# Optimization experiments

Measured on AMD Instinct MI355X. Metric: run time of the kernel, lower is better.

Reference implementation:

```python
import jax, jax.numpy as jnp
import numpy as np

B, C, CI, H, W = 8, 256, 128, 48, 48


def conv1x1(x, w, b):
    # x: (B,C,H,W), w: (CI,C), b: (CI,)
    return jnp.einsum('bchw,oc->bohw', x, w) + b[None, :, None, None]


def setup_inputs() -> dict:
    key = jax.random.key(0)
    ks = jax.random.split(key, 14)
    s = 1.0 / np.sqrt(C)
    d = {
        'x_1': jax.random.normal(ks[0], (B, C, H, W), jnp.float32),
        'x_2': jax.random.normal(ks[1], (B, C, H, W), jnp.float32),
    }
    names = ['v1', 'k1', 'q1', 'v2', 'k2', 'q2']
    for i, n in enumerate(names):
        d['w_' + n] = jax.random.uniform(ks[2 + 2 * i], (CI, C), jnp.float32, -s, s)
        d['b_' + n] = jax.random.uniform(ks[3 + 2 * i], (CI,), jnp.float32, -s, s)
    return d


def reference(x_1, x_2, w_v1, b_v1, w_k1, b_k1, w_q1, b_q1,
              w_v2, b_v2, w_k2, b_k2, w_q2, b_q2):
    b, ci, h, w = x_1.shape[0], w_v1.shape[0], x_1.shape[2], x_1.shape[3]
    n = h * w
    V1 = conv1x1(x_1, w_v1, b_v1).reshape(b, ci, n)
    K1 = conv1x1(x_1, w_k1, b_k1).reshape(b, ci, n)
    Q1 = conv1x1(x_1, w_q1, b_q1).reshape(b, ci, n)
    V2 = conv1x1(x_2, w_v2, b_v2).reshape(b, ci, n)
    K2 = conv1x1(x_2, w_k2, b_k2).reshape(b, ci, n)
    Q2 = conv1x1(x_2, w_q2, b_q2).reshape(b, ci, n)
    # sigmoid-gated cross attention, (B, N, N)
    R12 = jax.nn.sigmoid(jnp.einsum('bcn,bcm->bnm', Q1, K2))
    R21 = jax.nn.sigmoid(jnp.einsum('bcn,bcm->bnm', Q2, K1))
    Fu1 = jnp.einsum('bnm,bcm->bcn', R12, V2).reshape(b, ci, h, w)
    Fu2 = jnp.einsum('bnm,bcm->bcn', R21, V1).reshape(b, ci, h, w)
    y_1 = jnp.concatenate([x_1, Fu1], axis=1)
    y_2 = jnp.concatenate([x_2, Fu2], axis=1)
    return (y_1, y_2)
```

## Files before the change

kernel.cpp:

```cpp
#include <hip/hip_runtime.h>
#include <hip/hip_bf16.h>


typedef __bf16 bf16;
typedef __bf16 bf16x8 __attribute__((ext_vector_type(8)));
typedef __bf16 bf16x4 __attribute__((ext_vector_type(4)));
typedef float f32x4 __attribute__((ext_vector_type(4)));

#define NB 8
#define NC 256
#define NCI 128
#define NHW 2304
#define NT32 72
#define KPAD 136
#define VPAD 72

__global__ __launch_bounds__(256) void wconv_kernel(
    const float* __restrict__ w0, const float* __restrict__ w1,
    const float* __restrict__ w2, const float* __restrict__ w3,
    const float* __restrict__ w4, const float* __restrict__ w5,
    bf16* __restrict__ dst)
{
    int idx = (blockIdx.x * 256 + threadIdx.x) * 8;
    int m = idx >> 15;
    int off = idx & 32767;
    const float* w = (m == 0) ? w0 : (m == 1) ? w1 : (m == 2) ? w2
                   : (m == 3) ? w3 : (m == 4) ? w4 : w5;
    f32x4 a0 = *(const f32x4*)(w + off);
    f32x4 a1 = *(const f32x4*)(w + off + 4);
    bf16x8 o;
    #pragma unroll
    for (int j = 0; j < 4; ++j) { o[j] = (bf16)a0[j]; o[4 + j] = (bf16)a1[j]; }
    *(bf16x8*)(dst + idx) = o;
}

__global__ __launch_bounds__(256) void qkv_kernel(
    const float* __restrict__ x1, const float* __restrict__ x2,
    const bf16* __restrict__ wb,
    const float* __restrict__ bv1, const float* __restrict__ bk1, const float* __restrict__ bq1,
    const float* __restrict__ bv2, const float* __restrict__ bk2, const float* __restrict__ bq2,
    bf16* __restrict__ Qt, bf16* __restrict__ Kt, bf16* __restrict__ Vt,
    float* __restrict__ out)
{
    __shared__ __align__(16) bf16 Xt[32 * 264];

    int gid = blockIdx.x;
    int nt = gid % NT32;
    int s = (gid / NT32) & 1;
    int b = gid / (2 * NT32);
    int n0 = nt * 32;

    const float* x = s ? x2 : x1;
    const bf16* wv = wb + (size_t)(s * 3 + 0) * (NCI * NC);
    const bf16* wk = wb + (size_t)(s * 3 + 1) * (NCI * NC);
    const bf16* wq = wb + (size_t)(s * 3 + 2) * (NCI * NC);
    const float* bv = s ? bv2 : bv1;
    const float* bk = s ? bk2 : bk1;
    const float* bq = s ? bq2 : bq1;
    float* outy = out + (size_t)s * (NB * 384 * NHW);

    int tid = threadIdx.x;
    {
        int n_off = (tid & 3) * 8;
        int c0l = tid >> 2;
        #pragma unroll
        for (int i = 0; i < 4; ++i) {
            int c = c0l + i * 64;
            const float* src = x + ((size_t)(b * NC + c) * NHW + n0 + n_off);
            f32x4 a0 = *(const f32x4*)src;
            f32x4 a1 = *(const f32x4*)(src + 4);
            float* dsty = outy + ((size_t)(b * 384 + c) * NHW + n0 + n_off);
            *(f32x4*)dsty = a0;
            *(f32x4*)(dsty + 4) = a1;
            #pragma unroll
            for (int j = 0; j < 4; ++j) {
                Xt[(n_off + j) * 264 + c] = (bf16)a0[j];
                Xt[(n_off + 4 + j) * 264 + c] = (bf16)a1[j];
            }
        }
    }
    __syncthreads();

    int lane = tid & 63;
    int wid = tid >> 6;
    int row = lane & 15, quad = lane >> 4;
    int ci_base = wid * 32;

    f32x4 acc[3][2][2];
    #pragma unroll
    for (int t = 0; t < 3; ++t)
        #pragma unroll
        for (int mi = 0; mi < 2; ++mi)
            #pragma unroll
            for (int j = 0; j < 2; ++j)
                acc[t][mi][j] = (f32x4){0.f, 0.f, 0.f, 0.f};

    const bf16* wptr[3] = {wq, wk, wv};
    #pragma unroll
    for (int ks = 0; ks < 8; ++ks) {
        int c0 = ks * 32 + quad * 8;
        bf16x8 bfrag[2];
        #pragma unroll
        for (int j = 0; j < 2; ++j)
            bfrag[j] = *(const bf16x8*)&Xt[(j * 16 + row) * 264 + c0];
        #pragma unroll
        for (int t = 0; t < 3; ++t) {
            #pragma unroll
            for (int mi = 0; mi < 2; ++mi) {
                bf16x8 afrag = *(const bf16x8*)&wptr[t][(size_t)(ci_base + mi * 16 + row) * NC + c0];
                #pragma unroll
                for (int j = 0; j < 2; ++j)
                    acc[t][mi][j] = __builtin_amdgcn_mfma_f32_16x16x32_bf16(
                        afrag, bfrag[j], acc[t][mi][j], 0, 0, 0);
            }
        }
    }

    size_t qkbase = ((size_t)s * NB + b) * NHW * NCI;
    size_t vbase  = ((size_t)s * NB + b) * NCI * NHW;
    #pragma unroll
    for (int mi = 0; mi < 2; ++mi) {
        int ci0 = ci_base + mi * 16 + quad * 4;
        f32x4 bq4 = *(const f32x4*)&bq[ci0];
        f32x4 bk4 = *(const f32x4*)&bk[ci0];
        f32x4 bv4 = *(const f32x4*)&bv[ci0];
        #pragma unroll
        for (int j = 0; j < 2; ++j) {
            int n = n0 + j * 16 + row;
            bf16x4 pk;
            #pragma unroll
            for (int r = 0; r < 4; ++r) pk[r] = (bf16)(acc[0][mi][j][r] + bq4[r]);
            *(bf16x4*)&Qt[qkbase + (size_t)n * NCI + ci0] = pk;
            #pragma unroll
            for (int r = 0; r < 4; ++r) pk[r] = (bf16)(acc[1][mi][j][r] + bk4[r]);
            *(bf16x4*)&Kt[qkbase + (size_t)n * NCI + ci0] = pk;
            #pragma unroll
            for (int r = 0; r < 4; ++r)
                Vt[vbase + (size_t)(ci0 + r) * NHW + n] = (bf16)(acc[2][mi][j][r] + bv4[r]);
        }
    }
}

__global__ __launch_bounds__(256) void attn_kernel(
    const bf16* __restrict__ Qt, const bf16* __restrict__ Kt, const bf16* __restrict__ Vt,
    float* __restrict__ out)
{
    __shared__ __align__(16) bf16 KT[64 * KPAD];
    __shared__ __align__(16) bf16 VT[128 * VPAD];
    __shared__ __align__(16) bf16 P[4][16 * 72];

    int gid = blockIdx.x;
    int pair = (gid & 7) * 2 + ((gid >> 3) & 1);
    int nt = gid >> 4;
    int dir = pair & 1;
    int b = pair >> 1;
    int n0 = nt * 64;

    int tid = threadIdx.x;
    int lane = tid & 63, w = tid >> 6;
    int row = lane & 15, quad = lane >> 4;

    int sq = dir, skv = dir ^ 1;
    const bf16* q = Qt + ((size_t)sq  * NB + b) * (NHW * NCI);
    const bf16* k = Kt + ((size_t)skv * NB + b) * (NHW * NCI);
    const bf16* v = Vt + ((size_t)skv * NB + b) * (NCI * NHW);
    float* outy = out + (size_t)dir * (NB * 384 * NHW) + ((size_t)b * 384 + 256) * NHW;

    int kgoff[4], vgoff[4];
    bf16 *klp[4], *vlp[4];
    #pragma unroll
    for (int i = 0; i < 4; ++i) {
        int c = tid + i * 256;
        int kr = c >> 4, kc = c & 15;
        kgoff[i] = kr * NCI + kc * 8;
        klp[i] = &KT[kr * KPAD + kc * 8];
        int vr = c >> 3, vc = c & 7;
        vgoff[i] = vr * NHW + vc * 8;
        vlp[i] = &VT[vr * VPAD + vc * 8];
    }

    int nw = n0 + w * 16;
    bf16x8 qf[4];
    #pragma unroll
    for (int ks = 0; ks < 4; ++ks)
        qf[ks] = *(const bf16x8*)&q[(size_t)(nw + row) * NCI + ks * 32 + quad * 8];

    f32x4 o[8];
    #pragma unroll
    for (int ct = 0; ct < 8; ++ct) o[ct] = (f32x4){0.f, 0.f, 0.f, 0.f};

    bf16* Pw = P[w];

    bf16x8 kreg[4], vreg[4];
    #pragma unroll
    for (int i = 0; i < 4; ++i) {
        kreg[i] = *(const bf16x8*)(k + kgoff[i]);
        vreg[i] = *(const bf16x8*)(v + vgoff[i]);
    }

    for (int mt = 0; mt < 36; ++mt) {
        __syncthreads();
        #pragma unroll
        for (int i = 0; i < 4; ++i) {
            *(bf16x8*)klp[i] = kreg[i];
            *(bf16x8*)vlp[i] = vreg[i];
        }
        __syncthreads();
        if (mt < 35) {
            size_t ko = (size_t)(mt + 1) * 64 * NCI;
            int vo = (mt + 1) * 64;
            #pragma unroll
            for (int i = 0; i < 4; ++i) {
                kreg[i] = *(const bf16x8*)(k + ko + kgoff[i]);
                vreg[i] = *(const bf16x8*)(v + vo + vgoff[i]);
            }
        }
        f32x4 sacc[4];
        #pragma unroll
        for (int j = 0; j < 4; ++j) sacc[j] = (f32x4){0.f, 0.f, 0.f, 0.f};
        #pragma unroll
        for (int ks = 0; ks < 4; ++ks) {
            #pragma unroll
            for (int j = 0; j < 4; ++j) {
                bf16x8 kf = *(const bf16x8*)&KT[(j * 16 + row) * KPAD + ks * 32 + quad * 8];
                sacc[j] = __builtin_amdgcn_mfma_f32_16x16x32_bf16(qf[ks], kf, sacc[j], 0, 0, 0);
            }
        }
        #pragma unroll
        for (int j = 0; j < 4; ++j) {
            #pragma unroll
            for (int r = 0; r < 4; ++r) {
                float xv = sacc[j][r];
                float e = __expf(-xv);
                float p = __builtin_amdgcn_rcpf(1.0f + e);
                Pw[(quad * 4 + r) * 72 + j * 16 + row] = (bf16)p;
            }
        }
        #pragma unroll
        for (int ks = 0; ks < 2; ++ks) {
            bf16x8 af = *(const bf16x8*)&Pw[row * 72 + ks * 32 + quad * 8];
            #pragma unroll
            for (int ct = 0; ct < 8; ++ct) {
                bf16x8 vf = *(const bf16x8*)&VT[(ct * 16 + row) * VPAD + ks * 32 + quad * 8];
                o[ct] = __builtin_amdgcn_mfma_f32_16x16x32_bf16(af, vf, o[ct], 0, 0, 0);
            }
        }
    }

    int nbase = nw + quad * 4;
    #pragma unroll
    for (int ct = 0; ct < 8; ++ct) {
        int c = ct * 16 + row;
        *(f32x4*)&outy[(size_t)c * NHW + nbase] = o[ct];
    }
}

extern "C" void kernel_launch(void* const* d_in, const int* in_sizes, int n_in,
                              void* d_out, int out_size, void* d_ws, size_t ws_size,
                              hipStream_t stream) {
    const float* x1  = (const float*)d_in[0];
    const float* x2  = (const float*)d_in[1];
    const float* wv1 = (const float*)d_in[2];  const float* bv1 = (const float*)d_in[3];
    const float* wk1 = (const float*)d_in[4];  const float* bk1 = (const float*)d_in[5];
    const float* wq1 = (const float*)d_in[6];  const float* bq1 = (const float*)d_in[7];
    const float* wv2 = (const float*)d_in[8];  const float* bv2 = (const float*)d_in[9];
    const float* wk2 = (const float*)d_in[10]; const float* bk2 = (const float*)d_in[11];
    const float* wq2 = (const float*)d_in[12]; const float* bq2 = (const float*)d_in[13];
    float* out = (float*)d_out;

    size_t per = (size_t)2 * NB * NHW * NCI;
    bf16* Qt = (bf16*)d_ws;
    bf16* Kt = Qt + per;
    bf16* Vt = Kt + per;
    bf16* wb = Vt + per;

    wconv_kernel<<<dim3(96), dim3(256), 0, stream>>>(wv1, wk1, wq1, wv2, wk2, wq2, wb);

    qkv_kernel<<<dim3(NB * 2 * NT32), dim3(256), 0, stream>>>(
        x1, x2, wb, bv1, bk1, bq1, bv2, bk2, bq2, Qt, Kt, Vt, out);

    attn_kernel<<<dim3(NB * 2 * 36), dim3(256), 0, stream>>>(Qt, Kt, Vt, out);
}
```

Measured before the change: 246.4 us.

## Switch attention to 32x32x16 MFMA with two 32-row waves per block

The attention kernel moves from 16x16x32 to 32x32x16 bf16 MFMA tiles. Each block now has 2 waves of 32 query rows instead of 4 waves of 16, so each thread stages twice as many K/V chunks per tile. The larger MFMA tile cuts LDS fragment reads per FLOP but halves the waves per block, which may reduce latency hiding. The qkv kernel's x load is also reshaped to 4-wide f32 vectors over 8 iterations.

```diff
diff --git a/kernel.cpp b/kernel.cpp
--- a/kernel.cpp
+++ b/kernel.cpp
@@ -6,6 +6,7 @@
 typedef __bf16 bf16x8 __attribute__((ext_vector_type(8)));
 typedef __bf16 bf16x4 __attribute__((ext_vector_type(4)));
 typedef float f32x4 __attribute__((ext_vector_type(4)));
+typedef float f32x16 __attribute__((ext_vector_type(16)));
 
 #define NB 8
 #define NC 256
@@ -14,6 +15,7 @@
 #define NT32 72
 #define KPAD 136
 #define VPAD 72
+#define PPAD 72
 
 __global__ __launch_bounds__(256) void wconv_kernel(
     const float* __restrict__ w0, const float* __restrict__ w1,
@@ -61,22 +63,17 @@
 
     int tid = threadIdx.x;
     {
-        int n_off = (tid & 3) * 8;
-        int c0l = tid >> 2;
-        #pragma unroll
-        for (int i = 0; i < 4; ++i) {
-            int c = c0l + i * 64;
-            const float* src = x + ((size_t)(b * NC + c) * NHW + n0 + n_off);
-            f32x4 a0 = *(const f32x4*)src;
-            f32x4 a1 = *(const f32x4*)(src + 4);
-            float* dsty = outy + ((size_t)(b * 384 + c) * NHW + n0 + n_off);
-            *(f32x4*)dsty = a0;
-            *(f32x4*)(dsty + 4) = a1;
-            #pragma unroll
-            for (int j = 0; j < 4; ++j) {
-                Xt[(n_off + j) * 264 + c] = (bf16)a0[j];
-                Xt[(n_off + 4 + j) * 264 + c] = (bf16)a1[j];
-            }
+        int noff = (tid & 7) * 4;
+        int cbase = tid >> 3;
+        #pragma unroll
+        for (int i = 0; i < 8; ++i) {
+            int c = cbase + i * 32;
+            const float* src = x + ((size_t)(b * NC + c) * NHW + n0 + noff);
+            f32x4 a = *(const f32x4*)src;
+            *(f32x4*)(outy + ((size_t)(b * 384 + c) * NHW + n0 + noff)) = a;
+            #pragma unroll
+            for (int j = 0; j < 4; ++j)
+                Xt[(noff + j) * 264 + c] = (bf16)a[j];
         }
     }
     __syncthreads();
@@ -141,13 +138,13 @@
     }
 }
 
-__global__ __launch_bounds__(256) void attn_kernel(
+__global__ __launch_bounds__(128) void attn_kernel(
     const bf16* __restrict__ Qt, const bf16* __restrict__ Kt, const bf16* __restrict__ Vt,
     float* __restrict__ out)
 {
     __shared__ __align__(16) bf16 KT[64 * KPAD];
     __shared__ __align__(16) bf16 VT[128 * VPAD];
-    __shared__ __align__(16) bf16 P[4][16 * 72];
+    __shared__ __align__(16) bf16 P[2][32 * PPAD];
 
     int gid = blockIdx.x;
     int pair = (gid & 7) * 2 + ((gid >> 3) & 1);
@@ -158,7 +155,7 @@
 
     int tid = threadIdx.x;
     int lane = tid & 63, w = tid >> 6;
-    int row = lane & 15, quad = lane >> 4;
+    int l32 = lane & 31, h = lane >> 5;
 
     int sq = dir, skv = dir ^ 1;
     const bf16* q = Qt + ((size_t)sq  * NB + b) * (NHW * NCI);
@@ -166,92 +163,94 @@
     const bf16* v = Vt + ((size_t)skv * NB + b) * (NCI * NHW);
     float* outy = out + (size_t)dir * (NB * 384 * NHW) + ((size_t)b * 384 + 256) * NHW;
 
-    int kgoff[4], vgoff[4];
-    bf16 *klp[4], *vlp[4];
-    #pragma unroll
-    for (int i = 0; i < 4; ++i) {
-        int c = tid + i * 256;
-        int kr = c >> 4, kc = c & 15;
-        kgoff[i] = kr * NCI + kc * 8;
-        klp[i] = &KT[kr * KPAD + kc * 8];
-        int vr = c >> 3, vc = c & 7;
-        vgoff[i] = vr * NHW + vc * 8;
-        vlp[i] = &VT[vr * VPAD + vc * 8];
-    }
-
-    int nw = n0 + w * 16;
-    bf16x8 qf[4];
-    #pragma unroll
-    for (int ks = 0; ks < 4; ++ks)
-        qf[ks] = *(const bf16x8*)&q[(size_t)(nw + row) * NCI + ks * 32 + quad * 8];
-
-    f32x4 o[8];
-    #pragma unroll
-    for (int ct = 0; ct < 8; ++ct) o[ct] = (f32x4){0.f, 0.f, 0.f, 0.f};
+    int krow = tid >> 4, kch = tid & 15;
+    int vrow = tid >> 3, vch = tid & 7;
+
+    int nw = n0 + w * 32;
+    bf16x8 qf[8];
+    #pragma unroll
+    for (int ks = 0; ks < 8; ++ks)
+        qf[ks] = *(const bf16x8*)&q[(size_t)(nw + l32) * NCI + ks * 16 + h * 8];
+
+    f32x16 o[4];
+    #pragma unroll
+    for (int ct = 0; ct < 4; ++ct)
+        #pragma unroll
+        for (int r = 0; r < 16; ++r) o[ct][r] = 0.f;
 
     bf16* Pw = P[w];
 
-    bf16x8 kreg[4], vreg[4];
-    #pragma unroll
-    for (int i = 0; i < 4; ++i) {
-        kreg[i] = *(const bf16x8*)(k + kgoff[i]);
-        vreg[i] = *(const bf16x8*)(v + vgoff[i]);
+    bf16x8 kreg[8], vreg[8];
+    #pragma unroll
+    for (int i = 0; i < 8; ++i) {
+        kreg[i] = *(const bf16x8*)&k[(size_t)(krow + 8 * i) * NCI + kch * 8];
+        vreg[i] = *(const bf16x8*)&v[(size_t)(vrow + 16 * i) * NHW + vch * 8];
     }
 
     for (int mt = 0; mt < 36; ++mt) {
         __syncthreads();
         #pragma unroll
-        for (int i = 0; i < 4; ++i) {
-            *(bf16x8*)klp[i] = kreg[i];
-            *(bf16x8*)vlp[i] = vreg[i];
+        for (int i = 0; i < 8; ++i) {
+            *(bf16x8*)&KT[(krow + 8 * i) * KPAD + kch * 8] = kreg[i];
+            *(bf16x8*)&VT[(vrow + 16 * i) * VPAD + vch * 8] = vreg[i];
         }
         __syncthreads();
         if (mt < 35) {
             size_t ko = (size_t)(mt + 1) * 64 * NCI;
             int vo = (mt + 1) * 64;
             #pragma unroll
-            for (int i = 0; i < 4; ++i) {
-                kreg[i] = *(const bf16x8*)(k + ko + kgoff[i]);
-                vreg[i] = *(const bf16x8*)(v + vo + vgoff[i]);
-            }
-        }
-        f32x4 sacc[4];
-        #pragma unroll
-        for (int j = 0; j < 4; ++j) sacc[j] = (f32x4){0.f, 0.f, 0.f, 0.f};
-        #pragma unroll
-        for (int ks = 0; ks < 4; ++ks) {
-            #pragma unroll
-            for (int j = 0; j < 4; ++j) {
-                bf16x8 kf = *(const bf16x8*)&KT[(j * 16 + row) * KPAD + ks * 32 + quad * 8];
-                sacc[j] = __builtin_amdgcn_mfma_f32_16x16x32_bf16(qf[ks], kf, sacc[j], 0, 0, 0);
-            }
-        }
-        #pragma unroll
-        for (int j = 0; j < 4; ++j) {
-            #pragma unroll
-            for (int r = 0; r < 4; ++r) {
-                float xv = sacc[j][r];
-                float e = __expf(-xv);
-                float p = __builtin_amdgcn_rcpf(1.0f + e);
-                Pw[(quad * 4 + r) * 72 + j * 16 + row] = (bf16)p;
-            }
-        }
-        #pragma unroll
-        for (int ks = 0; ks < 2; ++ks) {
-            bf16x8 af = *(const bf16x8*)&Pw[row * 72 + ks * 32 + quad * 8];
-            #pragma unroll
-            for (int ct = 0; ct < 8; ++ct) {
-                bf16x8 vf = *(const bf16x8*)&VT[(ct * 16 + row) * VPAD + ks * 32 + quad * 8];
-                o[ct] = __builtin_amdgcn_mfma_f32_16x16x32_bf16(af, vf, o[ct], 0, 0, 0);
-            }
-        }
-    }
-
-    int nbase = nw + quad * 4;
-    #pragma unroll
-    for (int ct = 0; ct < 8; ++ct) {
-        int c = ct * 16 + row;
-        *(f32x4*)&outy[(size_t)c * NHW + nbase] = o[ct];
+            for (int i = 0; i < 8; ++i) {
+                kreg[i] = *(const bf16x8*)&k[ko + (size_t)(krow + 8 * i) * NCI + kch * 8];
+                vreg[i] = *(const bf16x8*)&v[(size_t)(vrow + 16 * i) * NHW + vo + vch * 8];
+            }
+        }
+        f32x16 sacc[2];
+        #pragma unroll
+        for (int j32 = 0; j32 < 2; ++j32)
+            #pragma unroll
+            for (int r = 0; r < 16; ++r) sacc[j32][r] = 0.f;
+        #pragma unroll
+        for (int ks = 0; ks < 8; ++ks) {
+            #pragma unroll
+            for (int j32 = 0; j32 < 2; ++j32) {
+                bf16x8 kf = *(const bf16x8*)&KT[(j32 * 32 + l32) * KPAD + ks * 16 + h * 8];
+                sacc[j32] = __builtin_amdgcn_mfma_f32_32x32x16_bf16(qf[ks], kf, sacc[j32], 0, 0, 0);
+            }
+        }
+        #pragma unroll
+        for (int j32 = 0; j32 < 2; ++j32) {
+            #pragma unroll
+            for (int g = 0; g < 4; ++g) {
+                #pragma unroll
+                for (int r = 0; r < 4; ++r) {
+                    float xv = sacc[j32][g * 4 + r];
+                    float e = __expf(-xv);
+                    float p = __builtin_amdgcn_rcpf(1.0f + e);
+                    Pw[(r + 8 * g + 4 * h) * PPAD + j32 * 32 + l32] = (bf16)p;
+                }
+            }
+        }
+        #pragma unroll
+        for (int ks2 = 0; ks2 < 4; ++ks2) {
+            bf16x8 af = *(const bf16x8*)&Pw[l32 * PPAD + ks2 * 16 + h * 8];
+            #pragma unroll
+            for (int ct = 0; ct < 4; ++ct) {
+                bf16x8 vf = *(const bf16x8*)&VT[(ct * 32 + l32) * VPAD + ks2 * 16 + h * 8];
+                o[ct] = __builtin_amdgcn_mfma_f32_32x32x16_bf16(af, vf, o[ct], 0, 0, 0);
+            }
+        }
+    }
+
+    #pragma unroll
+    for (int ct = 0; ct < 4; ++ct) {
+        int c = ct * 32 + l32;
+        #pragma unroll
+        for (int g = 0; g < 4; ++g) {
+            f32x4 pk;
+            #pragma unroll
+            for (int r = 0; r < 4; ++r) pk[r] = o[ct][g * 4 + r];
+            *(f32x4*)&outy[(size_t)c * NHW + nw + 8 * g + 4 * h] = pk;
+        }
     }
 }
 
@@ -279,5 +278,5 @@
     qkv_kernel<<<dim3(NB * 2 * NT32), dim3(256), 0, stream>>>(
         x1, x2, wb, bv1, bk1, bq1, bv2, bk2, bq2, Qt, Kt, Vt, out);
 
-    attn_kernel<<<dim3(NB * 2 * 36), dim3(256), 0, stream>>>(Qt, Kt, Vt, out);
-}
+    attn_kernel<<<dim3(NB * 2 * 36), dim3(128), 0, stream>>>(Qt, Kt, Vt, out);
+}
```

Result: slower. 256.4 us (+4.1%).
